# Optimization experiments

Measured on AMD Instinct MI355X. Metric: run time of the kernel, lower is better.

## Reference

```python
import jax, jax.numpy as jnp
import numpy as np

NUM_HEADS = 8
DIM_HEAD = 32


def setup_inputs() -> dict:
    key = jax.random.key(0)
    k1, k2, k3 = jax.random.split(key, 3)
    dim = 256
    inner = NUM_HEADS * DIM_HEAD  # 256
    x = jax.random.normal(k1, (2, dim, 32, 32, 32), dtype=jnp.float32)
    # Conv1d(kernel_size=1, bias=False) weights == plain matrices [out_ch, in_ch]
    w_qkv = jax.random.normal(k2, (inner * 3, dim), dtype=jnp.float32) * 0.02
    w_out = jax.random.normal(k3, (dim, inner), dtype=jnp.float32) * 0.02
    return {"x": x, "w_qkv": w_qkv, "w_out": w_out}


def reference(x, w_qkv, w_out):
    b, c, h, w, d = x.shape
    n = h * w * d
    x_flat = x.reshape(b, c, n)
    # 1x1 conv == channel matmul: [b, 3*inner, n]
    qkv = jnp.einsum('oc,bcn->bon', w_qkv, x_flat)
    q, k, v = jnp.split(qkv, 3, axis=1)

    def to_heads(t):  # [b, inner, n] -> [b, H, n, Dh]
        return t.reshape(b, NUM_HEADS, DIM_HEAD, n).transpose(0, 1, 3, 2)

    q = jax.nn.softmax(to_heads(q), axis=-1)   # softmax over dim_head
    k = jax.nn.softmax(to_heads(k), axis=-2)   # softmax over tokens n
    v = to_heads(v)
    # context: [b, H, Dh, Dh]
    context = jnp.einsum('bhnd,bhne->bhde', k, v)
    attn_out = jnp.einsum('bhnd,bhde->bhne', q, context)  # [b, H, n, Dh]
    attn_out = attn_out.transpose(0, 1, 3, 2).reshape(b, NUM_HEADS * DIM_HEAD, n)
    out = jnp.einsum('oi,bin->bon', w_out, attn_out)  # to_out 1x1 conv (dropout=0)
    return out.reshape(b, c, h, w, d)
```

## Files before the change

kernel.cpp:

```cpp
#include <hip/hip_runtime.h>

#define NTOK 32768

typedef __attribute__((ext_vector_type(8))) short  bf16x8;
typedef __attribute__((ext_vector_type(8))) unsigned short u16x8;
typedef __attribute__((ext_vector_type(4))) float  f32x4;

__device__ __forceinline__ unsigned short f32_to_bf16(float f) {
    unsigned int u = __float_as_uint(f);
    u += 0x7FFFu + ((u >> 16) & 1u);
    return (unsigned short)(u >> 16);
}
__device__ __forceinline__ float bf16_to_f32(unsigned short h) {
    return __uint_as_float(((unsigned int)h) << 16);
}

template <typename BT, typename CT, int MCHUNKS, bool QSOFT>
__global__ __launch_bounds__(256) void gemm_bstat(
    const unsigned short* __restrict__ A, const BT* __restrict__ B,
    CT* __restrict__ C, long sA, long sB, long sC)
{
    const int bz = blockIdx.y;
    A += (long)bz * sA; B += (long)bz * sB; C += (long)bz * sC;
    const int col0 = blockIdx.x * 128;

    __shared__ unsigned short Bs[128 * 256];

    const int t = threadIdx.x;
    const int wave = t >> 6, lane = t & 63;
    const int wm = wave >> 1, wn = wave & 1;
    const int m16 = lane & 15, quad = lane >> 4;

    {
        const int n = t & 127;
        const int kg0 = (t >> 7) * 16;
        const int key = n & 7;
        const BT* bcol = B + col0 + n;
        #pragma unroll
        for (int g = 0; g < 16; ++g) {
            const int kg = kg0 + g;
            unsigned short tmp[8];
            #pragma unroll
            for (int i = 0; i < 8; ++i) {
                BT v = bcol[(size_t)(kg * 8 + i) * NTOK];
                if constexpr (sizeof(BT) == 4) tmp[i] = f32_to_bf16((float)v);
                else                           tmp[i] = (unsigned short)v;
            }
            *(u16x8*)&Bs[n * 256 + ((kg ^ key) * 8)] = *(const u16x8*)tmp;
        }
    }
    __syncthreads();

    const int swk = m16 & 7;

    for (int mc = 0; mc < MCHUNKS; ++mc) {
        const int m0 = mc * 128;
        f32x4 acc[4][4] = {};

        const unsigned short* Abase = A + (size_t)(m0 + wm * 64 + m16) * 256 + quad * 8;

        #pragma unroll
        for (int kk = 0; kk < 8; ++kk) {
            bf16x8 bf[4];
            #pragma unroll
            for (int nt = 0; nt < 4; ++nt) {
                const int col = wn * 64 + nt * 16 + m16;
                bf[nt] = *(const bf16x8*)&Bs[col * 256 + (((kk * 4 + quad) ^ swk) * 8)];
            }
            #pragma unroll
            for (int mt = 0; mt < 4; ++mt) {
                const bf16x8 af = *(const bf16x8*)&Abase[(size_t)mt * 16 * 256 + kk * 32];
                #pragma unroll
                for (int nt = 0; nt < 4; ++nt)
                    acc[mt][nt] = __builtin_amdgcn_mfma_f32_16x16x32_bf16(
                        af, bf[nt], acc[mt][nt], 0, 0, 0);
            }
        }

        if (QSOFT && m0 < 256) {
            #pragma unroll
            for (int hj = 0; hj < 2; ++hj) {
                #pragma unroll
                for (int nt = 0; nt < 4; ++nt) {
                    float mx = -1e30f;
                    #pragma unroll
                    for (int p = 0; p < 2; ++p)
                        #pragma unroll
                        for (int r = 0; r < 4; ++r)
                            mx = fmaxf(mx, acc[hj * 2 + p][nt][r]);
                    mx = fmaxf(mx, __shfl_xor(mx, 16, 64));
                    mx = fmaxf(mx, __shfl_xor(mx, 32, 64));
                    float s = 0.f;
                    #pragma unroll
                    for (int p = 0; p < 2; ++p)
                        #pragma unroll
                        for (int r = 0; r < 4; ++r) {
                            const float e = __expf(acc[hj * 2 + p][nt][r] - mx);
                            acc[hj * 2 + p][nt][r] = e;
                            s += e;
                        }
                    s += __shfl_xor(s, 16, 64);
                    s += __shfl_xor(s, 32, 64);
                    const float inv = 1.0f / s;
                    #pragma unroll
                    for (int p = 0; p < 2; ++p)
                        #pragma unroll
                        for (int r = 0; r < 4; ++r)
                            acc[hj * 2 + p][nt][r] *= inv;
                }
            }
        }

        #pragma unroll
        for (int mt = 0; mt < 4; ++mt) {
            #pragma unroll
            for (int nt = 0; nt < 4; ++nt) {
                #pragma unroll
                for (int r = 0; r < 4; ++r) {
                    const int row = m0 + wm * 64 + mt * 16 + quad * 4 + r;
                    const int col = col0 + wn * 64 + nt * 16 + m16;
                    if constexpr (sizeof(CT) == 4)
                        C[(size_t)row * NTOK + col] = acc[mt][nt][r];
                    else
                        C[(size_t)row * NTOK + col] = f32_to_bf16(acc[mt][nt][r]);
                }
            }
        }
    }
}

__global__ __launch_bounds__(256) void cast_bf16_kernel(
    const float* __restrict__ src, unsigned short* __restrict__ dst, int n4)
{
    const int i = blockIdx.x * 256 + threadIdx.x;
    if (i < n4) {
        float4 v = ((const float4*)src)[i];
        ushort4 o;
        o.x = f32_to_bf16(v.x); o.y = f32_to_bf16(v.y);
        o.z = f32_to_bf16(v.z); o.w = f32_to_bf16(v.w);
        ((ushort4*)dst)[i] = o;
    }
}

#define CCHUNK 256
__global__ __launch_bounds__(512) void ctx_mfma_kernel(
    const unsigned short* __restrict__ qkv,
    float* __restrict__ num, float* __restrict__ den)
{
    const int b = blockIdx.y;
    const int n0 = blockIdx.x * CCHUNK;
    const int h = threadIdx.x >> 6;
    const int lane = threadIdx.x & 63;
    const int m16 = lane & 15, quad = lane >> 4;

    const unsigned short* kb =
        qkv + ((long)b * 768 + 256 + h * 32 + m16) * (long)NTOK + n0 + quad * 8;
    const unsigned short* vb =
        qkv + ((long)b * 768 + 512 + h * 32 + m16) * (long)NTOK + n0 + quad * 8;

    f32x4 acc[2][2] = {};
    float dp[2] = {0.f, 0.f};

    #pragma unroll
    for (int n = 0; n < CCHUNK; n += 32) {
        bf16x8 af[2], bfv[2];
        #pragma unroll
        for (int dt = 0; dt < 2; ++dt) {
            const u16x8 kr = *(const u16x8*)(kb + (size_t)dt * 16 * NTOK + n);
            unsigned short tmp[8];
            #pragma unroll
            for (int i = 0; i < 8; ++i) {
                const float e = __expf(bf16_to_f32(kr[i]));
                const unsigned short eb = f32_to_bf16(e);
                tmp[i] = eb;
                dp[dt] += bf16_to_f32(eb);
            }
            af[dt] = *(const bf16x8*)tmp;
        }
        #pragma unroll
        for (int et = 0; et < 2; ++et)
            bfv[et] = *(const bf16x8*)(vb + (size_t)et * 16 * NTOK + n);
        #pragma unroll
        for (int dt = 0; dt < 2; ++dt)
            #pragma unroll
            for (int et = 0; et < 2; ++et)
                acc[dt][et] = __builtin_amdgcn_mfma_f32_16x16x32_bf16(
                    af[dt], bfv[et], acc[dt][et], 0, 0, 0);
    }

    float* nbase = num + ((long)(b * 8 + h) * 32) * 32;
    #pragma unroll
    for (int dt = 0; dt < 2; ++dt)
        #pragma unroll
        for (int et = 0; et < 2; ++et)
            #pragma unroll
            for (int r = 0; r < 4; ++r)
                atomicAdd(&nbase[(dt * 16 + quad * 4 + r) * 32 + et * 16 + m16],
                          acc[dt][et][r]);

    #pragma unroll
    for (int dt = 0; dt < 2; ++dt) {
        float s = dp[dt];
        s += __shfl_xor(s, 16, 64);
        s += __shfl_xor(s, 32, 64);
        if (quad == 0)
            atomicAdd(&den[b * 256 + h * 32 + dt * 16 + m16], s);
    }
}

__global__ __launch_bounds__(256) void combine_kernel(
    const float* __restrict__ w_out, const float* __restrict__ num,
    const float* __restrict__ den, unsigned short* __restrict__ W2)
{
    const int tid = blockIdx.x * 256 + threadIdx.x;
    const int b = tid >> 16;
    const int rem = tid & 65535;
    const int o = rem >> 8;
    const int i = rem & 255;
    const int h = i >> 5, d = i & 31;
    const float* wrow = w_out + o * 256 + h * 32;
    const float* nrow = num + (((long)(b * 8 + h) * 32 + d) << 5);
    float s = 0.f;
    #pragma unroll
    for (int e = 0; e < 32; ++e) s += wrow[e] * nrow[e];
    W2[tid] = f32_to_bf16(s / den[b * 256 + h * 32 + d]);
}

extern "C" void kernel_launch(void* const* d_in, const int* in_sizes, int n_in,
                              void* d_out, int out_size, void* d_ws, size_t ws_size,
                              hipStream_t stream)
{
    const float* x     = (const float*)d_in[0];
    const float* w_qkv = (const float*)d_in[1];
    const float* w_out = (const float*)d_in[2];
    float* out = (float*)d_out;

    unsigned short* qkv_bf = (unsigned short*)d_ws;
    const long qkv_elems = 2L * 768 * NTOK;
    unsigned short* wqkv_bf = qkv_bf + qkv_elems;
    unsigned short* W2 = wqkv_bf + 768 * 256;
    float* num  = (float*)(W2 + 2 * 256 * 256);
    float* den  = num + 16384;

    hipMemsetAsync(num, 0, (16384 + 512) * sizeof(float), stream);

    cast_bf16_kernel<<<192, 256, 0, stream>>>(w_qkv, wqkv_bf, 768 * 256 / 4);

    gemm_bstat<float, unsigned short, 6, true><<<dim3(256, 2), 256, 0, stream>>>(
        wqkv_bf, x, qkv_bf, 0L, 256L * NTOK, 768L * NTOK);

    ctx_mfma_kernel<<<dim3(NTOK / CCHUNK, 2), 512, 0, stream>>>(qkv_bf, num, den);

    combine_kernel<<<512, 256, 0, stream>>>(w_out, num, den, W2);

    gemm_bstat<unsigned short, float, 2, false><<<dim3(256, 2), 256, 0, stream>>>(
        W2, qkv_bf, out, 65536L, 768L * NTOK, 256L * NTOK);
}
```

Baseline: 249.8 us.

## Use 512-thread GEMM blocks with swapped MFMA operands and vectorized stores

The GEMM kernel now runs 8 waves per block, each owning a 32x64 tile instead of 64x64. That halves accumulator registers and aims for more resident waves. The MFMA operand order is swapped so each lane holds 4 consecutive columns, which allows float4/ushort4 vector stores instead of scalar strided stores. The q-softmax is reworked to reduce across lanes within 16-lane groups under the new layout. The trade-off is that each wave issues more A loads from global memory for the same B tile.

```diff
diff --git a/kernel.cpp b/kernel.cpp
--- a/kernel.cpp
+++ b/kernel.cpp
@@ -16,7 +16,7 @@
 }
 
 template <typename BT, typename CT, int MCHUNKS, bool QSOFT>
-__global__ __launch_bounds__(256) void gemm_bstat(
+__global__ __launch_bounds__(512, 4) void gemm_bstat(
     const unsigned short* __restrict__ A, const BT* __restrict__ B,
     CT* __restrict__ C, long sA, long sB, long sC)
 {
@@ -33,11 +33,11 @@
 
     {
         const int n = t & 127;
-        const int kg0 = (t >> 7) * 16;
+        const int kg0 = (t >> 7) * 8;
         const int key = n & 7;
         const BT* bcol = B + col0 + n;
         #pragma unroll
-        for (int g = 0; g < 16; ++g) {
+        for (int g = 0; g < 8; ++g) {
             const int kg = kg0 + g;
             unsigned short tmp[8];
             #pragma unroll
@@ -55,9 +55,9 @@
 
     for (int mc = 0; mc < MCHUNKS; ++mc) {
         const int m0 = mc * 128;
-        f32x4 acc[4][4] = {};
-
-        const unsigned short* Abase = A + (size_t)(m0 + wm * 64 + m16) * 256 + quad * 8;
+        f32x4 acc[2][4] = {};
+
+        const unsigned short* Abase = A + (size_t)(m0 + wm * 32 + m16) * 256 + quad * 8;
 
         #pragma unroll
         for (int kk = 0; kk < 8; ++kk) {
@@ -68,61 +68,55 @@
                 bf[nt] = *(const bf16x8*)&Bs[col * 256 + (((kk * 4 + quad) ^ swk) * 8)];
             }
             #pragma unroll
-            for (int mt = 0; mt < 4; ++mt) {
+            for (int mt = 0; mt < 2; ++mt) {
                 const bf16x8 af = *(const bf16x8*)&Abase[(size_t)mt * 16 * 256 + kk * 32];
                 #pragma unroll
                 for (int nt = 0; nt < 4; ++nt)
                     acc[mt][nt] = __builtin_amdgcn_mfma_f32_16x16x32_bf16(
-                        af, bf[nt], acc[mt][nt], 0, 0, 0);
+                        bf[nt], af, acc[mt][nt], 0, 0, 0);
             }
         }
 
         if (QSOFT && m0 < 256) {
-            #pragma unroll
-            for (int hj = 0; hj < 2; ++hj) {
-                #pragma unroll
-                for (int nt = 0; nt < 4; ++nt) {
-                    float mx = -1e30f;
-                    #pragma unroll
-                    for (int p = 0; p < 2; ++p)
-                        #pragma unroll
-                        for (int r = 0; r < 4; ++r)
-                            mx = fmaxf(mx, acc[hj * 2 + p][nt][r]);
-                    mx = fmaxf(mx, __shfl_xor(mx, 16, 64));
-                    mx = fmaxf(mx, __shfl_xor(mx, 32, 64));
-                    float s = 0.f;
-                    #pragma unroll
-                    for (int p = 0; p < 2; ++p)
-                        #pragma unroll
-                        for (int r = 0; r < 4; ++r) {
-                            const float e = __expf(acc[hj * 2 + p][nt][r] - mx);
-                            acc[hj * 2 + p][nt][r] = e;
-                            s += e;
-                        }
-                    s += __shfl_xor(s, 16, 64);
-                    s += __shfl_xor(s, 32, 64);
-                    const float inv = 1.0f / s;
-                    #pragma unroll
-                    for (int p = 0; p < 2; ++p)
-                        #pragma unroll
-                        for (int r = 0; r < 4; ++r)
-                            acc[hj * 2 + p][nt][r] *= inv;
-                }
-            }
-        }
-
-        #pragma unroll
-        for (int mt = 0; mt < 4; ++mt) {
             #pragma unroll
             for (int nt = 0; nt < 4; ++nt) {
                 #pragma unroll
                 for (int r = 0; r < 4; ++r) {
-                    const int row = m0 + wm * 64 + mt * 16 + quad * 4 + r;
-                    const int col = col0 + wn * 64 + nt * 16 + m16;
-                    if constexpr (sizeof(CT) == 4)
-                        C[(size_t)row * NTOK + col] = acc[mt][nt][r];
-                    else
-                        C[(size_t)row * NTOK + col] = f32_to_bf16(acc[mt][nt][r]);
+                    float mx = fmaxf(acc[0][nt][r], acc[1][nt][r]);
+                    mx = fmaxf(mx, __shfl_xor(mx, 1, 64));
+                    mx = fmaxf(mx, __shfl_xor(mx, 2, 64));
+                    mx = fmaxf(mx, __shfl_xor(mx, 4, 64));
+                    mx = fmaxf(mx, __shfl_xor(mx, 8, 64));
+                    const float e0 = __expf(acc[0][nt][r] - mx);
+                    const float e1 = __expf(acc[1][nt][r] - mx);
+                    float s = e0 + e1;
+                    s += __shfl_xor(s, 1, 64);
+                    s += __shfl_xor(s, 2, 64);
+                    s += __shfl_xor(s, 4, 64);
+                    s += __shfl_xor(s, 8, 64);
+                    const float inv = 1.0f / s;
+                    acc[0][nt][r] = e0 * inv;
+                    acc[1][nt][r] = e1 * inv;
+                }
+            }
+        }
+
+        #pragma unroll
+        for (int mt = 0; mt < 2; ++mt) {
+            const int row = m0 + wm * 32 + mt * 16 + m16;
+            #pragma unroll
+            for (int nt = 0; nt < 4; ++nt) {
+                const int col = col0 + wn * 64 + nt * 16 + quad * 4;
+                if constexpr (sizeof(CT) == 4) {
+                    *(float4*)&C[(size_t)row * NTOK + col] =
+                        *(const float4*)&acc[mt][nt];
+                } else {
+                    ushort4 o;
+                    o.x = f32_to_bf16(acc[mt][nt][0]);
+                    o.y = f32_to_bf16(acc[mt][nt][1]);
+                    o.z = f32_to_bf16(acc[mt][nt][2]);
+                    o.w = f32_to_bf16(acc[mt][nt][3]);
+                    *(ushort4*)&C[(size_t)row * NTOK + col] = o;
                 }
             }
         }
@@ -246,13 +240,13 @@
 
     cast_bf16_kernel<<<192, 256, 0, stream>>>(w_qkv, wqkv_bf, 768 * 256 / 4);
 
-    gemm_bstat<float, unsigned short, 6, true><<<dim3(256, 2), 256, 0, stream>>>(
+    gemm_bstat<float, unsigned short, 6, true><<<dim3(256, 2), 512, 0, stream>>>(
         wqkv_bf, x, qkv_bf, 0L, 256L * NTOK, 768L * NTOK);
 
     ctx_mfma_kernel<<<dim3(NTOK / CCHUNK, 2), 512, 0, stream>>>(qkv_bf, num, den);
 
     combine_kernel<<<512, 256, 0, stream>>>(w_out, num, den, W2);
 
-    gemm_bstat<unsigned short, float, 2, false><<<dim3(256, 2), 256, 0, stream>>>(
+    gemm_bstat<unsigned short, float, 2, false><<<dim3(256, 2), 512, 0, stream>>>(
         W2, qkv_bf, out, 65536L, 768L * NTOK, 256L * NTOK);
 }
```

After: 296.2 us. 1.19x slower.
